# Optimization experiments

Hardware: AMD Instinct MI355X
Metric: run time of the kernel (lower is better)

Reference implementation:

```python
import jax, jax.numpy as jnp
import numpy as np

EMB = 512
HEADS = 8
HD = EMB // HEADS
DEPTH = 6
CONT = 100
CAT_DIMS = [100] * 28
CAT = len(CAT_DIMS)
HID = int(EMB * (4.0 / 3.0))  # 682, FT-Transformer ReGLU hidden
B = 128
OFFSETS = jnp.asarray(np.concatenate([[0], np.cumsum(CAT_DIMS[:-1])]).astype(np.int32))
SQRT_EMB = float(np.sqrt(EMB))  # scores are DIVIDED by emb**-0.5 in the source


def setup_inputs() -> dict:
    key = jax.random.key(0)
    ks = jax.random.split(key, 16)
    s = 0.02
    x_cat = jax.random.randint(ks[0], (B, CAT), 0, CAT_DIMS[0]).astype(jnp.float32)
    x_cont = jax.random.normal(ks[1], (B, CONT), dtype=jnp.float32)
    x = jnp.concatenate([x_cat, x_cont], axis=1)  # [B, CAT+CONT]
    return {
        "x": x,
        "tok_w": jax.random.normal(ks[2], (CONT + 1, EMB)) * s,
        "tok_b": jax.random.normal(ks[3], (CONT + CAT, EMB)) * s,
        "cat_emb": jax.random.normal(ks[4], (sum(CAT_DIMS), EMB)) * s,
        "Wqkv": jax.random.normal(ks[5], (DEPTH, EMB, 3 * EMB)) * s,
        "bqkv": jnp.zeros((DEPTH, 3 * EMB)),
        "Wout": jax.random.normal(ks[6], (DEPTH, EMB, EMB)) * s,
        "bout": jnp.zeros((DEPTH, EMB)),
        "W0": jax.random.normal(ks[7], (DEPTH, EMB, 2 * HID)) * s,
        "b0": jnp.zeros((DEPTH, 2 * HID)),
        "W1": jax.random.normal(ks[8], (DEPTH, HID, EMB)) * s,
        "b1": jnp.zeros((DEPTH, EMB)),
        "ln0_g": jnp.ones((DEPTH, EMB)),
        "ln0_b": jnp.zeros((DEPTH, EMB)),
        "ln1_g": jnp.ones((DEPTH, EMB)),
        "ln1_b": jnp.zeros((DEPTH, EMB)),
    }


def _ln(x, g, b):
    m = x.mean(-1, keepdims=True)
    v = x.var(-1, keepdims=True)
    return (x - m) / jnp.sqrt(v + 1e-5) * g + b


def _attn(x, Wqkv, bqkv, Wout, bout):
    Bn, S, _ = x.shape
    # faithful layout: reshape to (B,S,H,3*hd), move heads, chunk last dim
    qkv = (x @ Wqkv + bqkv).reshape(Bn, S, HEADS, 3 * HD).transpose(0, 2, 1, 3)
    q, k, v = jnp.split(qkv, 3, axis=-1)  # each [B,H,S,hd]
    scores = jnp.einsum("bhqd,bhkd->bhqk", q, k) * SQRT_EMB  # / (emb**-0.5)
    attn = jax.nn.softmax(jax.nn.softmax(scores, axis=-1), axis=-1)  # double softmax, as in source
    o = jnp.einsum("bhqk,bhkd->bhqd", attn, v)
    o = o.transpose(0, 2, 1, 3).reshape(Bn, S, EMB)
    return o @ Wout + bout


def _reglu(x):
    a, b = jnp.split(x, 2, axis=-1)
    return a * jax.nn.relu(b)


def _forward(x, tok_w, tok_b, cat_emb, Wqkv, bqkv, Wout, bout, W0, b0, W1, b1,
             ln0_g, ln0_b, ln1_g, ln1_b):
    # --- feature tokenizer ---
    x_cats = x[:, :CAT].astype(jnp.int32)
    x_conts = jnp.concatenate([jnp.ones((x.shape[0], 1), x.dtype), x[:, CAT:]], axis=1)  # [B, CONT+1]
    h = tok_w[None] * x_conts[:, :, None]  # [B, CONT+1, EMB]
    h = jnp.concatenate([h, cat_emb[x_cats + OFFSETS[None]]], axis=1)  # [B, S=129, EMB]
    bias = jnp.concatenate([jnp.zeros((1, EMB), h.dtype), tok_b], axis=0)
    h = h + bias[None]
    # --- transformer stack ---
    for i in range(DEPTH):
        xin = _ln(h, ln0_g[i], ln0_b[i]) if i else h  # layer 0 has no norm0
        h = h + _attn(xin, Wqkv[i], bqkv[i], Wout[i], bout[i])
        r = _ln(h, ln1_g[i], ln1_b[i])
        r = _reglu(r @ W0[i] + b0[i]) @ W1[i] + b1[i]
        h = h + r
    return h[:, 0]  # CLS token


def reference(x, tok_w, tok_b, cat_emb, Wqkv, bqkv, Wout, bout, W0, b0, W1, b1,
              ln0_g, ln0_b, ln1_g, ln1_b):
    return _forward(x, tok_w, tok_b, cat_emb, Wqkv, bqkv, Wout, bout, W0, b0, W1, b1,
                    ln0_g, ln0_b, ln1_g, ln1_b)
```

## Files before the change

kernel.cpp:

```cpp
#include <hip/hip_runtime.h>
#include <hip/hip_bf16.h>
#include <stdint.h>


typedef __hip_bfloat16 bf16_t;
typedef __attribute__((ext_vector_type(8))) __bf16 bf16x8;
typedef __attribute__((ext_vector_type(4))) __bf16 bf16x4;
typedef __attribute__((ext_vector_type(2))) __bf16 bf16x2;
typedef __attribute__((ext_vector_type(4))) float floatx4;

constexpr int M_ROWS = 16512;
constexpr float SQRT_EMB_F = 22.627416997969522f;

__device__ __forceinline__ floatx4 mfma16(bf16x8 a, bf16x8 b, floatx4 c) {
  return __builtin_amdgcn_mfma_f32_16x16x32_bf16(a, b, c, 0, 0, 0);
}

__device__ __forceinline__ void gload_lds16(const bf16_t* g, bf16_t* l) {
  __builtin_amdgcn_global_load_lds(
      (const __attribute__((address_space(1))) void*)g,
      (__attribute__((address_space(3))) void*)l, 16, 0, 0);
}

__device__ __forceinline__ size_t frag_chunk(int m, int k, int KT) {
  return ((size_t)(m >> 4) * KT + (k >> 5)) * 512 + (m & 15) * 8 + 128 * ((k >> 3) & 3);
}
__device__ __forceinline__ size_t frag_elem(int m, int k, int KT) {
  return frag_chunk(m, k, KT) + (k & 7);
}

template <int PERM>
__global__ __launch_bounds__(256) void transpose_cvt(const float* __restrict__ W,
    bf16_t* __restrict__ WT, int K, int N, int KP, int NP)
{
  __shared__ float tile[32][33];
  int k0 = blockIdx.x * 32, n0 = blockIdx.y * 32;
  const float* Wl = W + (size_t)blockIdx.z * K * N;
  bf16_t* WTl = WT + (size_t)blockIdx.z * NP * KP;
  const int KT = KP >> 5;
  #pragma unroll
  for (int r = 0; r < 32; r += 8) {
    int k = k0 + threadIdx.y + r, n = n0 + threadIdx.x;
    int srcn = PERM ? ((n & 1) ? 682 + (n >> 1) : (n >> 1)) : n;
    int valid = (k < K) && (PERM ? (n < 1364) : (n < N));
    tile[threadIdx.y + r][threadIdx.x] = valid ? Wl[(size_t)k * N + srcn] : 0.f;
  }
  __syncthreads();
  #pragma unroll
  for (int r = 0; r < 32; r += 8) {
    int n = n0 + threadIdx.y + r, k = k0 + threadIdx.x;
    if (n < NP && k < KP)
      WTl[frag_elem(n, k, KT)] = __float2bfloat16(tile[threadIdx.x][threadIdx.y + r]);
  }
}

__global__ __launch_bounds__(256) void tokenizer_kernel(const float* __restrict__ x,
    const float* __restrict__ tok_w, const float* __restrict__ tok_b,
    const float* __restrict__ cat_emb, float* __restrict__ h, bf16_t* __restrict__ ab)
{
  int row = blockIdx.x * 4 + (threadIdx.x >> 6);
  int lane = threadIdx.x & 63, e0 = lane * 8;
  int b = row / 129, t = row - b * 129;
  float v[8];
  if (t == 0) {
    #pragma unroll
    for (int u = 0; u < 8; u++) v[u] = tok_w[e0 + u];
  } else if (t <= 100) {
    float xv = x[(size_t)b * 128 + 28 + (t - 1)];
    const float* wp = tok_w + (size_t)t * 512 + e0;
    const float* bp = tok_b + (size_t)(t - 1) * 512 + e0;
    #pragma unroll
    for (int u = 0; u < 8; u++) v[u] = wp[u] * xv + bp[u];
  } else {
    int j = t - 101;
    int idx = (int)x[(size_t)b * 128 + j] + 100 * j;
    const float* cp = cat_emb + (size_t)idx * 512 + e0;
    const float* bp = tok_b + (size_t)(t - 1) * 512 + e0;
    #pragma unroll
    for (int u = 0; u < 8; u++) v[u] = cp[u] + bp[u];
  }
  float* hr = h + (size_t)row * 512 + e0;
  #pragma unroll
  for (int u = 0; u < 8; u++) hr[u] = v[u];
  bf16x8 o8;
  #pragma unroll
  for (int u = 0; u < 8; u++) o8[u] = (__bf16)__float2bfloat16(v[u]);
  *(bf16x8*)(ab + ((size_t)(row >> 4) * 16 + (lane >> 2)) * 512 + (row & 15) * 8 + 128 * (lane & 3)) = o8;
}

__global__ __launch_bounds__(256) void ln_kernel(const float* __restrict__ hin,
    bf16_t* __restrict__ out, const float* __restrict__ g, const float* __restrict__ bta)
{
  int row = blockIdx.x * 4 + (threadIdx.x >> 6);
  int lane = threadIdx.x & 63;
  const float* hr = hin + (size_t)row * 512 + lane * 8;
  float4 v0 = *(const float4*)hr;
  float4 v1 = *(const float4*)(hr + 4);
  float s = v0.x + v0.y + v0.z + v0.w + v1.x + v1.y + v1.z + v1.w;
  float q = v0.x * v0.x + v0.y * v0.y + v0.z * v0.z + v0.w * v0.w
          + v1.x * v1.x + v1.y * v1.y + v1.z * v1.z + v1.w * v1.w;
  #pragma unroll
  for (int o = 1; o < 64; o <<= 1) { s += __shfl_xor(s, o); q += __shfl_xor(q, o); }
  float mean = s * (1.f / 512.f);
  float var = q * (1.f / 512.f) - mean * mean;
  float rstd = rsqrtf(var + 1e-5f);
  float4 g0 = *(const float4*)(g + lane * 8);
  float4 g1 = *(const float4*)(g + lane * 8 + 4);
  float4 b0v = *(const float4*)(bta + lane * 8);
  float4 b1v = *(const float4*)(bta + lane * 8 + 4);
  bf16x8 o8;
  o8[0] = (__bf16)__float2bfloat16((v0.x - mean) * rstd * g0.x + b0v.x);
  o8[1] = (__bf16)__float2bfloat16((v0.y - mean) * rstd * g0.y + b0v.y);
  o8[2] = (__bf16)__float2bfloat16((v0.z - mean) * rstd * g0.z + b0v.z);
  o8[3] = (__bf16)__float2bfloat16((v0.w - mean) * rstd * g0.w + b0v.w);
  o8[4] = (__bf16)__float2bfloat16((v1.x - mean) * rstd * g1.x + b1v.x);
  o8[5] = (__bf16)__float2bfloat16((v1.y - mean) * rstd * g1.y + b1v.y);
  o8[6] = (__bf16)__float2bfloat16((v1.z - mean) * rstd * g1.z + b1v.z);
  o8[7] = (__bf16)__float2bfloat16((v1.w - mean) * rstd * g1.w + b1v.w);
  *(bf16x8*)(out + ((size_t)(row >> 4) * 16 + (lane >> 2)) * 512 + (row & 15) * 8 + 128 * (lane & 3)) = o8;
}

template <int MODE>
__global__ __launch_bounds__(256, 4) void gemm_frag(const bf16_t* __restrict__ A,
    const bf16_t* __restrict__ BT, const float* __restrict__ bias, int biasN,
    const float* __restrict__ resid, void* __restrict__ outp, int K, int N)
{
  __shared__ bf16_t lsB[2][8][512];

  const int total = gridDim.x * gridDim.y;
  const int lin = blockIdx.y * gridDim.x + blockIdx.x;
  const int xcd = lin & 7, kb2 = lin >> 3;
  const int qch = total >> 3, rch = total & 7;
  const int idx = xcd * qch + (xcd < rch ? xcd : rch) + kb2;
  const int bm = idx / gridDim.x;
  const int bn = idx - bm * gridDim.x;
  const int m0 = bm * 128, n0 = bn * 128;

  const int tid = threadIdx.x;
  const int w = tid >> 6, l = tid & 63, l15 = l & 15, quad = l >> 4;
  const int wm = (w >> 1) * 64, wn = (w & 1) * 64;
  const int KT = K >> 5;

  const bf16_t* pa[4];
  #pragma unroll
  for (int i = 0; i < 4; i++)
    pa[i] = A + ((size_t)((m0 >> 4) + (w >> 1) * 4 + i) * KT) * 512 + l * 8;

  const bf16_t* gB0 = BT + ((size_t)((n0 >> 4) + 2 * w) * KT) * 512 + l * 8;
  const bf16_t* gB1 = gB0 + (size_t)KT * 512;
  const int sb = w * 2;
  const int rb = (w & 1) * 4;

  auto stageB = [&](int buf, int t) {
    const size_t go = (size_t)t * 512;
    gload_lds16(gB0 + go, &lsB[buf][sb][0]);
    gload_lds16(gB1 + go, &lsB[buf][sb + 1][0]);
  };

  floatx4 z4 = {0.f, 0.f, 0.f, 0.f};
  floatx4 acc[4][4];
  #pragma unroll
  for (int i = 0; i < 4; i++)
    #pragma unroll
    for (int j = 0; j < 4; j++) acc[i][j] = z4;

  bf16x8 af[4];
  #pragma unroll
  for (int i = 0; i < 4; i++) af[i] = *(const bf16x8*)pa[i];
  stageB(0, 0);
  __syncthreads();

  int cur = 0;
  for (int t = 0; t < KT; ++t) {
    if (t + 1 < KT) stageB(cur ^ 1, t + 1);
    bf16x8 bg[4];
    #pragma unroll
    for (int j = 0; j < 4; j++) bg[j] = *(const bf16x8*)&lsB[cur][rb + j][l * 8];
    #pragma unroll
    for (int i = 0; i < 4; i++) {
      #pragma unroll
      for (int j = 0; j < 4; j++)
        acc[i][j] = mfma16(bg[j], af[i], acc[i][j]);
      if (t + 1 < KT)
        af[i] = *(const bf16x8*)(pa[i] + (size_t)(t + 1) * 512);
    }
    __syncthreads();
    cur ^= 1;
  }

  #pragma unroll
  for (int i = 0; i < 4; i++) {
    int m = m0 + wm + i * 16 + l15;
    #pragma unroll
    for (int j = 0; j < 4; j++) {
      int nb = n0 + wn + j * 16 + quad * 4;
      if (MODE == 2) {
        int c2b = nb >> 1;
        bf16x2 o2;
        #pragma unroll
        for (int u = 0; u < 2; u++) {
          int c2 = c2b + u;
          bool vld = (2 * c2 < biasN);
          float av = acc[i][j][2 * u]     + (vld ? bias[c2] : 0.f);
          float bv = acc[i][j][2 * u + 1] + (vld ? bias[682 + c2] : 0.f);
          o2[u] = (__bf16)__float2bfloat16(av * fmaxf(bv, 0.f));
        }
        *(bf16x2*)&((bf16_t*)outp)[frag_elem(m, c2b, (N >> 1) >> 5)] = o2;
      } else if (MODE == 1) {
        size_t idx2 = (size_t)m * N + nb;
        float4 rv = *(const float4*)(resid + idx2);
        float4 ov;
        ov.x = acc[i][j][0] + bias[nb + 0] + rv.x;
        ov.y = acc[i][j][1] + bias[nb + 1] + rv.y;
        ov.z = acc[i][j][2] + bias[nb + 2] + rv.z;
        ov.w = acc[i][j][3] + bias[nb + 3] + rv.w;
        *(float4*)((float*)outp + idx2) = ov;
      } else {
        bf16x4 o4;
        #pragma unroll
        for (int r = 0; r < 4; r++) {
          float bv = (nb + r < biasN) ? bias[nb + r] : 0.f;
          o4[r] = (__bf16)__float2bfloat16(acc[i][j][r] + bv);
        }
        *(bf16x4*)&((bf16_t*)outp)[frag_elem(m, nb, N >> 5)] = o4;
      }
    }
  }
}

constexpr int SP = 160;
__global__ __launch_bounds__(256) void attn_kernel(const bf16_t* __restrict__ qkv,
                                                   bf16_t* __restrict__ attnout)
{
  __shared__ bf16_t vt_lds[64 * SP];
  __shared__ float sc[32 * SP];
  bf16_t* p_lds = (bf16_t*)sc;
  __bf16* vt_raw = (__bf16*)vt_lds;

  const int bh = blockIdx.x, b = bh >> 3, hh = bh & 7;
  const int tid = threadIdx.x;
  const int w = tid >> 6, l = tid & 63, l15 = l & 15, quad = l >> 4;
  const int rbase = b * 129;

  for (int i = tid; i < SP * 64 / 2; i += 256) ((unsigned int*)vt_lds)[i] = 0u;
  __syncthreads();
  for (int c = tid; c < 129 * 8; c += 256) {
    int s = c >> 3, ch = c & 7;
    bf16x8 tv = *(const bf16x8*)(qkv + frag_chunk(rbase + s, hh * 192 + 128 + ch * 8, 48));
    #pragma unroll
    for (int j = 0; j < 8; j++) vt_raw[(size_t)(ch * 8 + j) * SP + s] = tv[j];
  }
  __syncthreads();

  for (int qt = 0; qt < 5; qt++) {
    bf16x8 zq = {};
    bf16x8 aq[2][2];
    #pragma unroll
    for (int mt = 0; mt < 2; mt++) {
      int m = qt * 32 + mt * 16 + l15;
      #pragma unroll
      for (int t = 0; t < 2; t++)
        aq[mt][t] = (m < 129)
            ? *(const bf16x8*)(qkv + frag_chunk(rbase + m, hh * 192 + t * 32 + quad * 8, 48)) : zq;
    }
    for (int nt = w; nt < 10; nt += 4) {
      int krow = nt * 16 + l15;
      floatx4 a0 = {0.f, 0.f, 0.f, 0.f}, a1 = {0.f, 0.f, 0.f, 0.f};
      #pragma unroll
      for (int t = 0; t < 2; t++) {
        bf16x8 kf = (krow < 129)
            ? *(const bf16x8*)(qkv + frag_chunk(rbase + krow, hh * 192 + 64 + t * 32 + quad * 8, 48))
            : zq;
        a0 = mfma16(aq[0][t], kf, a0);
        a1 = mfma16(aq[1][t], kf, a1);
      }
      #pragma unroll
      for (int r = 0; r < 4; r++) {
        sc[(quad * 4 + r) * SP + nt * 16 + l15]      = a0[r] * SQRT_EMB_F;
        sc[(16 + quad * 4 + r) * SP + nt * 16 + l15] = a1[r] * SQRT_EMB_F;
      }
    }
    __syncthreads();

    {
      int row = tid >> 3, sub = tid & 7;
      float vv[20];
      float mx = -1e30f;
      #pragma unroll
      for (int c = 0; c < 20; c++) {
        int j = sub + c * 8;
        vv[c] = (j < 129) ? sc[row * SP + j] : -1e30f;
        mx = fmaxf(mx, vv[c]);
      }
      #pragma unroll
      for (int o = 1; o < 8; o <<= 1) mx = fmaxf(mx, __shfl_xor(mx, o, 8));
      float sum = 0.f;
      #pragma unroll
      for (int c = 0; c < 20; c++) {
        int j = sub + c * 8;
        vv[c] = (j < 129) ? __expf(vv[c] - mx) : 0.f;
        sum += vv[c];
      }
      #pragma unroll
      for (int o = 1; o < 8; o <<= 1) sum += __shfl_xor(sum, o, 8);
      float inv = 1.f / sum;
      float mx2 = 0.f;
      #pragma unroll
      for (int c = 0; c < 20; c++) { vv[c] *= inv; mx2 = fmaxf(mx2, vv[c]); }
      #pragma unroll
      for (int o = 1; o < 8; o <<= 1) mx2 = fmaxf(mx2, __shfl_xor(mx2, o, 8));
      float sum2 = 0.f;
      #pragma unroll
      for (int c = 0; c < 20; c++) {
        int j = sub + c * 8;
        vv[c] = (j < 129) ? __expf(vv[c] - mx2) : 0.f;
        sum2 += vv[c];
      }
      #pragma unroll
      for (int o = 1; o < 8; o <<= 1) sum2 += __shfl_xor(sum2, o, 8);
      float inv2 = 1.f / sum2;
      __syncthreads();
      #pragma unroll
      for (int c = 0; c < 20; c++) {
        int j = sub + c * 8;
        p_lds[row * SP + j] = __float2bfloat16(vv[c] * inv2);
      }
    }
    __syncthreads();

    {
      int mt = w >> 1, nt0 = (w & 1) * 2;
      floatx4 oacc[2];
      oacc[0] = floatx4{0.f, 0.f, 0.f, 0.f};
      oacc[1] = floatx4{0.f, 0.f, 0.f, 0.f};
      #pragma unroll
      for (int t = 0; t < 5; t++) {
        bf16x8 pf = *(const bf16x8*)&p_lds[(mt * 16 + l15) * SP + t * 32 + quad * 8];
        #pragma unroll
        for (int n = 0; n < 2; n++) {
          bf16x8 vf = *(const bf16x8*)&vt_lds[((nt0 + n) * 16 + l15) * SP + t * 32 + quad * 8];
          oacc[n] = mfma16(pf, vf, oacc[n]);
        }
      }
      #pragma unroll
      for (int n = 0; n < 2; n++)
        #pragma unroll
        for (int r = 0; r < 4; r++) {
          int sq = qt * 32 + mt * 16 + quad * 4 + r;
          if (sq < 129) {
            int cc = hh * 64 + (nt0 + n) * 16 + l15;
            attnout[frag_elem(rbase + sq, cc, 16)] = __float2bfloat16(oacc[n][r]);
          }
        }
    }
    __syncthreads();
  }
}

__global__ __launch_bounds__(256) void out_copy(const float* __restrict__ h,
                                                float* __restrict__ out)
{
  int b = blockIdx.x, e = threadIdx.x;
  out[(size_t)b * 512 + e]       = h[(size_t)b * 129 * 512 + e];
  out[(size_t)b * 512 + e + 256] = h[(size_t)b * 129 * 512 + e + 256];
}

extern "C" void kernel_launch(void* const* d_in, const int* in_sizes, int n_in,
                              void* d_out, int out_size, void* d_ws, size_t ws_size,
                              hipStream_t stream)
{
  const float* x       = (const float*)d_in[0];
  const float* tok_w   = (const float*)d_in[1];
  const float* tok_b   = (const float*)d_in[2];
  const float* cat_emb = (const float*)d_in[3];
  const float* Wqkv    = (const float*)d_in[4];
  const float* bqkv    = (const float*)d_in[5];
  const float* Wout    = (const float*)d_in[6];
  const float* bout    = (const float*)d_in[7];
  const float* W0      = (const float*)d_in[8];
  const float* b0      = (const float*)d_in[9];
  const float* W1      = (const float*)d_in[10];
  const float* b1      = (const float*)d_in[11];
  const float* ln0_g   = (const float*)d_in[12];
  const float* ln0_b   = (const float*)d_in[13];
  const float* ln1_g   = (const float*)d_in[14];
  const float* ln1_b   = (const float*)d_in[15];

  size_t off = 0;
  char* base = (char*)d_ws;
  auto alloc = [&](size_t n) { char* p = base + off; off += (n + 255) & ~(size_t)255; return p; };
  float*  h     = (float*) alloc((size_t)M_ROWS * 512 * 4);
  bf16_t* ab    = (bf16_t*)alloc((size_t)M_ROWS * 512 * 2);
  bf16_t* qkv   = (bf16_t*)alloc((size_t)M_ROWS * 1536 * 2);
  bf16_t* attno = (bf16_t*)alloc((size_t)M_ROWS * 512 * 2);
  bf16_t* regl  = (bf16_t*)alloc((size_t)M_ROWS * 704 * 2);
  bf16_t* WqkvT = (bf16_t*)alloc((size_t)6 * 1536 * 512 * 2);
  bf16_t* WoutT = (bf16_t*)alloc((size_t)6 * 512 * 512 * 2);
  bf16_t* W0T   = (bf16_t*)alloc((size_t)6 * 1408 * 512 * 2);
  bf16_t* W1T   = (bf16_t*)alloc((size_t)6 * 512 * 704 * 2);
  (void)ws_size; (void)in_sizes; (void)n_in; (void)out_size;

  dim3 tb(32, 8, 1);
  transpose_cvt<0><<<dim3(16, 48, 6), tb, 0, stream>>>(Wqkv, WqkvT, 512, 1536, 512, 1536);
  transpose_cvt<0><<<dim3(16, 16, 6), tb, 0, stream>>>(Wout, WoutT, 512, 512, 512, 512);
  transpose_cvt<1><<<dim3(16, 44, 6), tb, 0, stream>>>(W0, W0T, 512, 1364, 512, 1408);
  transpose_cvt<0><<<dim3(22, 16, 6), tb, 0, stream>>>(W1, W1T, 682, 512, 704, 512);

  tokenizer_kernel<<<M_ROWS / 4, 256, 0, stream>>>(x, tok_w, tok_b, cat_emb, h, ab);

  for (int i = 0; i < 6; i++) {
    if (i)
      ln_kernel<<<M_ROWS / 4, 256, 0, stream>>>(h, ab, ln0_g + (size_t)i * 512,
                                                ln0_b + (size_t)i * 512);
    gemm_frag<0><<<dim3(12, 129), 256, 0, stream>>>(
        ab, WqkvT + (size_t)i * 1536 * 512, bqkv + (size_t)i * 1536, 1536, nullptr, qkv, 512, 1536);
    attn_kernel<<<1024, 256, 0, stream>>>(qkv, attno);
    gemm_frag<1><<<dim3(4, 129), 256, 0, stream>>>(
        attno, WoutT + (size_t)i * 512 * 512, bout + (size_t)i * 512, 512, h, h, 512, 512);
    ln_kernel<<<M_ROWS / 4, 256, 0, stream>>>(h, ab, ln1_g + (size_t)i * 512,
                                              ln1_b + (size_t)i * 512);
    gemm_frag<2><<<dim3(11, 129), 256, 0, stream>>>(
        ab, W0T + (size_t)i * 1408 * 512, b0 + (size_t)i * 1364, 1364, nullptr, regl, 512, 1408);
    gemm_frag<1><<<dim3(4, 129), 256, 0, stream>>>(
        regl, W1T + (size_t)i * 512 * 704, b1 + (size_t)i * 512, 512, h, h, 704, 512);
  }

  out_copy<<<128, 256, 0, stream>>>(h, (float*)d_out);
}
```

Baseline: 1.290 ms.

## Fuse residual-add GEMMs with following LayerNorm via full-row tiles

Replaces the N=512 residual GEMMs and the separate LayerNorm kernels with a gemm_ln kernel where each 512-thread block owns 32 full rows. It computes bias plus residual, writes h, reduces row statistics across waves in LDS, and emits the normalized bf16 A operand for the next GEMM. The last layer writes the CLS rows straight to the output, dropping the out_copy kernel. This removes separate LN launches and the extra reads of h. The cost is a GEMM that loads operands directly from global memory without LDS staging, and far fewer blocks (516).

```diff
diff --git a/kernel.cpp b/kernel.cpp
--- a/kernel.cpp
+++ b/kernel.cpp
@@ -86,38 +86,6 @@
   #pragma unroll
   for (int u = 0; u < 8; u++) o8[u] = (__bf16)__float2bfloat16(v[u]);
   *(bf16x8*)(ab + ((size_t)(row >> 4) * 16 + (lane >> 2)) * 512 + (row & 15) * 8 + 128 * (lane & 3)) = o8;
-}
-
-__global__ __launch_bounds__(256) void ln_kernel(const float* __restrict__ hin,
-    bf16_t* __restrict__ out, const float* __restrict__ g, const float* __restrict__ bta)
-{
-  int row = blockIdx.x * 4 + (threadIdx.x >> 6);
-  int lane = threadIdx.x & 63;
-  const float* hr = hin + (size_t)row * 512 + lane * 8;
-  float4 v0 = *(const float4*)hr;
-  float4 v1 = *(const float4*)(hr + 4);
-  float s = v0.x + v0.y + v0.z + v0.w + v1.x + v1.y + v1.z + v1.w;
-  float q = v0.x * v0.x + v0.y * v0.y + v0.z * v0.z + v0.w * v0.w
-          + v1.x * v1.x + v1.y * v1.y + v1.z * v1.z + v1.w * v1.w;
-  #pragma unroll
-  for (int o = 1; o < 64; o <<= 1) { s += __shfl_xor(s, o); q += __shfl_xor(q, o); }
-  float mean = s * (1.f / 512.f);
-  float var = q * (1.f / 512.f) - mean * mean;
-  float rstd = rsqrtf(var + 1e-5f);
-  float4 g0 = *(const float4*)(g + lane * 8);
-  float4 g1 = *(const float4*)(g + lane * 8 + 4);
-  float4 b0v = *(const float4*)(bta + lane * 8);
-  float4 b1v = *(const float4*)(bta + lane * 8 + 4);
-  bf16x8 o8;
-  o8[0] = (__bf16)__float2bfloat16((v0.x - mean) * rstd * g0.x + b0v.x);
-  o8[1] = (__bf16)__float2bfloat16((v0.y - mean) * rstd * g0.y + b0v.y);
-  o8[2] = (__bf16)__float2bfloat16((v0.z - mean) * rstd * g0.z + b0v.z);
-  o8[3] = (__bf16)__float2bfloat16((v0.w - mean) * rstd * g0.w + b0v.w);
-  o8[4] = (__bf16)__float2bfloat16((v1.x - mean) * rstd * g1.x + b1v.x);
-  o8[5] = (__bf16)__float2bfloat16((v1.y - mean) * rstd * g1.y + b1v.y);
-  o8[6] = (__bf16)__float2bfloat16((v1.z - mean) * rstd * g1.z + b1v.z);
-  o8[7] = (__bf16)__float2bfloat16((v1.w - mean) * rstd * g1.w + b1v.w);
-  *(bf16x8*)(out + ((size_t)(row >> 4) * 16 + (lane >> 2)) * 512 + (row & 15) * 8 + 128 * (lane & 3)) = o8;
 }
 
 template <int MODE>
@@ -206,15 +174,6 @@
           o2[u] = (__bf16)__float2bfloat16(av * fmaxf(bv, 0.f));
         }
         *(bf16x2*)&((bf16_t*)outp)[frag_elem(m, c2b, (N >> 1) >> 5)] = o2;
-      } else if (MODE == 1) {
-        size_t idx2 = (size_t)m * N + nb;
-        float4 rv = *(const float4*)(resid + idx2);
-        float4 ov;
-        ov.x = acc[i][j][0] + bias[nb + 0] + rv.x;
-        ov.y = acc[i][j][1] + bias[nb + 1] + rv.y;
-        ov.z = acc[i][j][2] + bias[nb + 2] + rv.z;
-        ov.w = acc[i][j][3] + bias[nb + 3] + rv.w;
-        *(float4*)((float*)outp + idx2) = ov;
       } else {
         bf16x4 o4;
         #pragma unroll
@@ -223,6 +182,128 @@
           o4[r] = (__bf16)__float2bfloat16(acc[i][j][r] + bv);
         }
         *(bf16x4*)&((bf16_t*)outp)[frag_elem(m, nb, N >> 5)] = o4;
+      }
+    }
+  }
+  (void)resid;
+}
+
+template <int DOLN, int DOOUT>
+__global__ __launch_bounds__(512, 4) void gemm_ln(const bf16_t* __restrict__ A,
+    const bf16_t* __restrict__ BT, const float* __restrict__ bias,
+    const float* __restrict__ resid, float* __restrict__ hout,
+    const float* __restrict__ g, const float* __restrict__ beta,
+    bf16_t* __restrict__ ab, float* __restrict__ outp, int K)
+{
+  __shared__ float lnred[2][8][32];
+
+  const int nwg = gridDim.x;
+  const int lin = blockIdx.x;
+  const int xcd = lin & 7, kb2 = lin >> 3;
+  const int qch = nwg >> 3, rch = nwg & 7;
+  const int idx = xcd * qch + (xcd < rch ? xcd : rch) + kb2;
+  const int m0 = idx * 32;
+
+  const int tid = threadIdx.x;
+  const int w = tid >> 6, l = tid & 63, l15 = l & 15, quad = l >> 4;
+  const int wn = w * 64;
+  const int KT = K >> 5;
+
+  const bf16_t* pa0 = A + ((size_t)(m0 >> 4) * KT) * 512 + l * 8;
+  const bf16_t* pa1 = pa0 + (size_t)KT * 512;
+  const bf16_t* pb[4];
+  #pragma unroll
+  for (int j = 0; j < 4; j++)
+    pb[j] = BT + ((size_t)((wn >> 4) + j) * KT) * 512 + l * 8;
+
+  floatx4 acc[2][4];
+  #pragma unroll
+  for (int i = 0; i < 2; i++)
+    #pragma unroll
+    for (int j = 0; j < 4; j++) acc[i][j] = floatx4{0.f, 0.f, 0.f, 0.f};
+
+  bf16x8 af0 = *(const bf16x8*)pa0;
+  bf16x8 af1 = *(const bf16x8*)pa1;
+  bf16x8 bg[4];
+  #pragma unroll
+  for (int j = 0; j < 4; j++) bg[j] = *(const bf16x8*)pb[j];
+
+  for (int t = 0; t < KT; ++t) {
+    #pragma unroll
+    for (int j = 0; j < 4; j++) {
+      acc[0][j] = mfma16(bg[j], af0, acc[0][j]);
+      acc[1][j] = mfma16(bg[j], af1, acc[1][j]);
+      if (t + 1 < KT) bg[j] = *(const bf16x8*)(pb[j] + (size_t)(t + 1) * 512);
+    }
+    if (t + 1 < KT) {
+      af0 = *(const bf16x8*)(pa0 + (size_t)(t + 1) * 512);
+      af1 = *(const bf16x8*)(pa1 + (size_t)(t + 1) * 512);
+    }
+  }
+
+  const int colb = wn + quad * 4;
+  float s[2] = {0.f, 0.f}, q[2] = {0.f, 0.f};
+  #pragma unroll
+  for (int i = 0; i < 2; i++) {
+    const int m = m0 + i * 16 + l15;
+    float* hr = hout + (size_t)m * 512;
+    const float* rr = resid + (size_t)m * 512;
+    #pragma unroll
+    for (int j = 0; j < 4; j++) {
+      const int nb = colb + j * 16;
+      float4 rv = *(const float4*)(rr + nb);
+      float4 bv = *(const float4*)(bias + nb);
+      floatx4 hv;
+      hv[0] = acc[i][j][0] + bv.x + rv.x;
+      hv[1] = acc[i][j][1] + bv.y + rv.y;
+      hv[2] = acc[i][j][2] + bv.z + rv.z;
+      hv[3] = acc[i][j][3] + bv.w + rv.w;
+      acc[i][j] = hv;
+      float4 hw = {hv[0], hv[1], hv[2], hv[3]};
+      *(float4*)(hr + nb) = hw;
+      if (DOOUT) {
+        if (m % 129 == 0)
+          *(float4*)(outp + (size_t)(m / 129) * 512 + nb) = hw;
+      }
+      s[i] += hv[0] + hv[1] + hv[2] + hv[3];
+      q[i] += hv[0] * hv[0] + hv[1] * hv[1] + hv[2] * hv[2] + hv[3] * hv[3];
+    }
+  }
+
+  if (DOLN) {
+    #pragma unroll
+    for (int i = 0; i < 2; i++) {
+      s[i] += __shfl_xor(s[i], 16); s[i] += __shfl_xor(s[i], 32);
+      q[i] += __shfl_xor(q[i], 16); q[i] += __shfl_xor(q[i], 32);
+    }
+    if (quad == 0) {
+      lnred[0][w][l15]      = s[0];  lnred[1][w][l15]      = q[0];
+      lnred[0][w][16 + l15] = s[1];  lnred[1][w][16 + l15] = q[1];
+    }
+    __syncthreads();
+    #pragma unroll
+    for (int i = 0; i < 2; i++) {
+      const int m = m0 + i * 16 + l15;
+      float ss = 0.f, qq = 0.f;
+      #pragma unroll
+      for (int wv = 0; wv < 8; wv++) {
+        ss += lnred[0][wv][i * 16 + l15];
+        qq += lnred[1][wv][i * 16 + l15];
+      }
+      float mean = ss * (1.f / 512.f);
+      float var = qq * (1.f / 512.f) - mean * mean;
+      float rstd = rsqrtf(var + 1e-5f);
+      #pragma unroll
+      for (int j = 0; j < 4; j++) {
+        const int nb = colb + j * 16;
+        float4 gg = *(const float4*)(g + nb);
+        float4 bb = *(const float4*)(beta + nb);
+        bf16x4 o4;
+        o4[0] = (__bf16)__float2bfloat16((acc[i][j][0] - mean) * rstd * gg.x + bb.x);
+        o4[1] = (__bf16)__float2bfloat16((acc[i][j][1] - mean) * rstd * gg.y + bb.y);
+        o4[2] = (__bf16)__float2bfloat16((acc[i][j][2] - mean) * rstd * gg.z + bb.z);
+        o4[3] = (__bf16)__float2bfloat16((acc[i][j][3] - mean) * rstd * gg.w + bb.w);
+        *(bf16x4*)&ab[frag_elem(m, nb, 16)] = o4;
       }
     }
   }
@@ -355,14 +436,6 @@
     }
     __syncthreads();
   }
-}
-
-__global__ __launch_bounds__(256) void out_copy(const float* __restrict__ h,
-                                                float* __restrict__ out)
-{
-  int b = blockIdx.x, e = threadIdx.x;
-  out[(size_t)b * 512 + e]       = h[(size_t)b * 129 * 512 + e];
-  out[(size_t)b * 512 + e + 256] = h[(size_t)b * 129 * 512 + e + 256];
 }
 
 extern "C" void kernel_launch(void* const* d_in, const int* in_sizes, int n_in,
@@ -408,22 +481,23 @@
 
   tokenizer_kernel<<<M_ROWS / 4, 256, 0, stream>>>(x, tok_w, tok_b, cat_emb, h, ab);
 
+  const int GLN = M_ROWS / 32;
   for (int i = 0; i < 6; i++) {
-    if (i)
-      ln_kernel<<<M_ROWS / 4, 256, 0, stream>>>(h, ab, ln0_g + (size_t)i * 512,
-                                                ln0_b + (size_t)i * 512);
     gemm_frag<0><<<dim3(12, 129), 256, 0, stream>>>(
         ab, WqkvT + (size_t)i * 1536 * 512, bqkv + (size_t)i * 1536, 1536, nullptr, qkv, 512, 1536);
     attn_kernel<<<1024, 256, 0, stream>>>(qkv, attno);
-    gemm_frag<1><<<dim3(4, 129), 256, 0, stream>>>(
-        attno, WoutT + (size_t)i * 512 * 512, bout + (size_t)i * 512, 512, h, h, 512, 512);
-    ln_kernel<<<M_ROWS / 4, 256, 0, stream>>>(h, ab, ln1_g + (size_t)i * 512,
-                                              ln1_b + (size_t)i * 512);
+    gemm_ln<1, 0><<<GLN, 512, 0, stream>>>(
+        attno, WoutT + (size_t)i * 512 * 512, bout + (size_t)i * 512, h, h,
+        ln1_g + (size_t)i * 512, ln1_b + (size_t)i * 512, ab, nullptr, 512);
     gemm_frag<2><<<dim3(11, 129), 256, 0, stream>>>(
         ab, W0T + (size_t)i * 1408 * 512, b0 + (size_t)i * 1364, 1364, nullptr, regl, 512, 1408);
-    gemm_frag<1><<<dim3(4, 129), 256, 0, stream>>>(
-        regl, W1T + (size_t)i * 512 * 704, b1 + (size_t)i * 512, 512, h, h, 704, 512);
-  }
-
-  out_copy<<<128, 256, 0, stream>>>(h, (float*)d_out);
-}
+    if (i < 5)
+      gemm_ln<1, 0><<<GLN, 512, 0, stream>>>(
+          regl, W1T + (size_t)i * 512 * 704, b1 + (size_t)i * 512, h, h,
+          ln0_g + (size_t)(i + 1) * 512, ln0_b + (size_t)(i + 1) * 512, ab, nullptr, 704);
+    else
+      gemm_ln<0, 1><<<GLN, 512, 0, stream>>>(
+          regl, W1T + (size_t)i * 512 * 704, b1 + (size_t)i * 512, h, h,
+          nullptr, nullptr, nullptr, (float*)d_out, 704);
+  }
+}
```

Result: no change. 1.305 ms (+1.2%).
